# Optimization experiments

Hardware: AMD Instinct MI355X
Metric: run time of the kernel (lower is better)

## Reference

```python
import jax, jax.numpy as jnp
import numpy as np

B, N, H, T = 64, 64, 128, 128


def setup_inputs() -> dict:
    key = jax.random.key(0)
    ks = jax.random.split(key, 8)
    tf = jax.random.normal(ks[0], (B, N, H, T), dtype=jnp.float32)
    # learnable symmetric adjacency parameter
    ap = jax.random.normal(ks[1], (N, N), dtype=jnp.float32) * 0.1
    ap = (ap + ap.T) / 2
    # edge MLP params (stored as (in, out) for x @ W)
    W1 = jax.random.normal(ks[2], (2 * H, H), dtype=jnp.float32) * (1.0 / np.sqrt(2 * H))
    b1 = jnp.zeros((H,), dtype=jnp.float32)
    W2 = jax.random.normal(ks[3], (H, H // 2), dtype=jnp.float32) * (1.0 / np.sqrt(H))
    b2 = jnp.zeros((H // 2,), dtype=jnp.float32)
    W3 = jax.random.normal(ks[4], (H // 2, 1), dtype=jnp.float32) * (1.0 / np.sqrt(H // 2))
    b3 = jnp.zeros((1,), dtype=jnp.float32)
    return {"temporal_features": tf, "adj_param": ap, "W1": W1, "b1": b1,
            "W2": W2, "b2": b2, "W3": W3, "b3": b3}


def reference(temporal_features, adj_param, W1, b1, W2, b2, W3, b3):
    # node features: mean over time -> (B, N, H)
    node = temporal_features.mean(axis=-1)
    h_dim = node.shape[-1]
    # concat([h_i, h_j]) @ W1 == h_i @ W1[:H] + h_j @ W1[H:]  (avoids materializing 2H concat)
    Wi, Wj = W1[:h_dim], W1[h_dim:]
    pi = jnp.einsum('bnh,hk->bnk', node, Wi)  # (B, N, H)
    pj = jnp.einsum('bnh,hk->bnk', node, Wj)
    h = jax.nn.relu(pi[:, :, None, :] + pj[:, None, :, :] + b1)  # (B, N, N, H)
    # Dropout(0.2) is identity at inference
    h = jax.nn.relu(jnp.einsum('bijh,hk->bijk', h, W2) + b2)      # (B, N, N, H//2)
    feat_adj = (jnp.einsum('bijk,ko->bijo', h, W3) + b3)[..., 0]  # (B, N, N)
    # combined method
    adj = 0.5 * adj_param[None, :, :] + 0.5 * feat_adj
    # symmetrize + relu
    adj = jax.nn.relu((adj + jnp.swapaxes(adj, -2, -1)) / 2)
    # add self-loops and degree-normalize rows
    adj = adj + jnp.eye(adj.shape[-1], dtype=adj.dtype)[None]
    adj = adj / (adj.sum(axis=-1, keepdims=True) + 1e-8)
    return adj
```

## Files before the change

### kernel.cpp

```cpp
#include <hip/hip_runtime.h>
#include <stdint.h>
#include <stddef.h>

typedef __attribute__((ext_vector_type(8))) short short8;
typedef __attribute__((ext_vector_type(4))) float f32x4;

__device__ inline unsigned short f2bf(float x) {
    unsigned u = __float_as_uint(x);
    unsigned r = (u + 0x7fffu + ((u >> 16) & 1u)) >> 16;
    return (unsigned short)r;
}

__global__ __launch_bounds__(256) void k1_mean(const float* __restrict__ tf,
                                               float* __restrict__ node) {
    int wave = (blockIdx.x * blockDim.x + threadIdx.x) >> 6;
    int lane = threadIdx.x & 63;
    int half = lane >> 5;
    int c = lane & 31;
    const float4* tf4 = reinterpret_cast<const float4*>(tf);
    size_t base = (size_t)wave * 8 * 64;

    float4 v[8];
#pragma unroll
    for (int k = 0; k < 8; ++k) v[k] = tf4[base + (size_t)k * 64 + lane];

    float s[8];
#pragma unroll
    for (int k = 0; k < 8; ++k) s[k] = (v[k].x + v[k].y) + (v[k].z + v[k].w);
#pragma unroll
    for (int m = 1; m <= 16; m <<= 1) {
#pragma unroll
        for (int k = 0; k < 8; ++k) s[k] += __shfl_xor(s[k], m);
    }
    if (c == 0) {
#pragma unroll
        for (int k = 0; k < 8; ++k) {
            int rp = wave * 8 + k;
            node[(size_t)rp * 2 + half] = s[k] * (1.0f / 128.0f);
        }
    }
}

__global__ __launch_bounds__(256) void k2_proj(const float* __restrict__ node,
                                               const float* __restrict__ W1,
                                               const float* __restrict__ b1,
                                               float* __restrict__ pi,
                                               float* __restrict__ pj) {
    const int LP = 136;
    __shared__ unsigned short A_lds[32 * LP];
    __shared__ unsigned short BT[128 * LP];
    __shared__ float b1s[128];

    int tid = threadIdx.x;
    int rblk = blockIdx.x >> 1;
    int half = blockIdx.x & 1;
    int r0 = rblk * 32;

    {
        int row = tid >> 3;
        int c0 = (tid & 7) * 16;
        const float4* src = reinterpret_cast<const float4*>(node + (size_t)(r0 + row) * 128 + c0);
        short8 pk[2];
#pragma unroll
        for (int q = 0; q < 2; ++q) {
            float4 va = src[q * 2 + 0];
            float4 vb = src[q * 2 + 1];
            pk[q][0] = (short)f2bf(va.x); pk[q][1] = (short)f2bf(va.y);
            pk[q][2] = (short)f2bf(va.z); pk[q][3] = (short)f2bf(va.w);
            pk[q][4] = (short)f2bf(vb.x); pk[q][5] = (short)f2bf(vb.y);
            pk[q][6] = (short)f2bf(vb.z); pk[q][7] = (short)f2bf(vb.w);
        }
        short8* dst = reinterpret_cast<short8*>(&A_lds[row * LP + c0]);
        dst[0] = pk[0];
        dst[1] = pk[1];
    }
    {
        int n = tid & 127;
        int kh = tid >> 7;
        const float* Wbase = W1 + (size_t)half * 128 * 128 + n;
#pragma unroll
        for (int g = 0; g < 8; ++g) {
            int kb = kh * 64 + g * 8;
            short8 pk;
#pragma unroll
            for (int e = 0; e < 8; ++e) pk[e] = (short)f2bf(Wbase[(size_t)(kb + e) * 128]);
            *reinterpret_cast<short8*>(&BT[n * LP + kb]) = pk;
        }
    }
    if (tid < 128) b1s[tid] = b1[tid];
    __syncthreads();

    int w = tid >> 6;
    int l = tid & 63;
    int lr = l & 15;
    int lg = l >> 4;
    int rt = w & 1;
    int ch = w >> 1;

    f32x4 acc[4] = {{0,0,0,0},{0,0,0,0},{0,0,0,0},{0,0,0,0}};
#pragma unroll
    for (int ks = 0; ks < 4; ++ks) {
        int kb = ks * 32 + lg * 8;
        short8 afrag = *reinterpret_cast<const short8*>(&A_lds[(rt * 16 + lr) * LP + kb]);
#pragma unroll
        for (int nt = 0; nt < 4; ++nt) {
            short8 bfrag = *reinterpret_cast<const short8*>(&BT[(ch * 64 + nt * 16 + lr) * LP + kb]);
            acc[nt] = __builtin_amdgcn_mfma_f32_16x16x32_bf16(afrag, bfrag, acc[nt], 0, 0, 0);
        }
    }
    float* out = half ? pj : pi;
#pragma unroll
    for (int nt = 0; nt < 4; ++nt) {
        int col = ch * 64 + nt * 16 + lr;
        float bias = half ? 0.0f : b1s[col];
#pragma unroll
        for (int r = 0; r < 4; ++r) {
            int row = r0 + rt * 16 + lg * 4 + r;
            out[(size_t)row * 128 + col] = acc[nt][r] + bias;
        }
    }
}

__global__ __launch_bounds__(256) void k3_mlp(const float* __restrict__ pi,
                                              const float* __restrict__ pj,
                                              const float* __restrict__ W2,
                                              const float* __restrict__ b2,
                                              const float* __restrict__ W3,
                                              const float* __restrict__ b3,
                                              float* __restrict__ F) {
    const int LDA = 136;
    __shared__ unsigned short A_lds[64 * LDA];
    __shared__ unsigned short W2T[64 * LDA];
    __shared__ float pipb4[4][128];
    __shared__ float b2s[64], w3s[64];

    int tid = threadIdx.x;
    int b = blockIdx.x >> 4;
    int it = blockIdx.x & 15;
    int i0 = it * 4;
    int jt = tid >> 2;
    int kq = tid & 3;

    float pjreg[32];
    {
        const float* src = pj + ((size_t)(b * 64 + jt) * 128 + kq * 32);
#pragma unroll
        for (int e = 0; e < 8; ++e) {
            float4 v = reinterpret_cast<const float4*>(src)[e];
            pjreg[e * 4 + 0] = v.x;
            pjreg[e * 4 + 1] = v.y;
            pjreg[e * 4 + 2] = v.z;
            pjreg[e * 4 + 3] = v.w;
        }
    }
    if (tid < 128) {
        int row = tid >> 5;
        int c4 = tid & 31;
        float4 v = reinterpret_cast<const float4*>(pi + ((size_t)(b * 64 + i0 + row) * 128))[c4];
        reinterpret_cast<float4*>(&pipb4[row][0])[c4] = v;
    }
    {
        int m = jt;
        for (int e = 0; e < 32; ++e) {
            int k = kq * 32 + e;
            W2T[m * LDA + k] = f2bf(W2[(size_t)k * 64 + m]);
        }
    }
    if (tid < 64) {
        b2s[tid] = b2[tid];
        w3s[tid] = W3[tid];
    }
    float b3v = b3[0];
    __syncthreads();

    int w = tid >> 6;
    int l = tid & 63;
    int lr = l & 15;
    int lg = l >> 4;

    for (int il = 0; il < 4; ++il) {
        {
            unsigned* dst = reinterpret_cast<unsigned*>(&A_lds[jt * LDA + kq * 32]);
#pragma unroll
            for (int e2 = 0; e2 < 16; ++e2) {
                float a0 = pipb4[il][kq * 32 + e2 * 2 + 0] + pjreg[e2 * 2 + 0];
                float a1 = pipb4[il][kq * 32 + e2 * 2 + 1] + pjreg[e2 * 2 + 1];
                a0 = fmaxf(a0, 0.0f);
                a1 = fmaxf(a1, 0.0f);
                dst[e2] = (unsigned)f2bf(a0) | ((unsigned)f2bf(a1) << 16);
            }
        }
        __syncthreads();
        f32x4 acc0 = {0.f, 0.f, 0.f, 0.f};
        f32x4 acc1 = {0.f, 0.f, 0.f, 0.f};
        f32x4 acc2 = {0.f, 0.f, 0.f, 0.f};
        f32x4 acc3 = {0.f, 0.f, 0.f, 0.f};
#pragma unroll
        for (int ks = 0; ks < 4; ++ks) {
            int kb = ks * 32 + lg * 8;
            short8 afrag = *reinterpret_cast<const short8*>(&A_lds[(w * 16 + lr) * LDA + kb]);
            short8 b0 = *reinterpret_cast<const short8*>(&W2T[(0 * 16 + lr) * LDA + kb]);
            short8 b1f = *reinterpret_cast<const short8*>(&W2T[(1 * 16 + lr) * LDA + kb]);
            short8 b2f = *reinterpret_cast<const short8*>(&W2T[(2 * 16 + lr) * LDA + kb]);
            short8 b3f = *reinterpret_cast<const short8*>(&W2T[(3 * 16 + lr) * LDA + kb]);
            acc0 = __builtin_amdgcn_mfma_f32_16x16x32_bf16(afrag, b0, acc0, 0, 0, 0);
            acc1 = __builtin_amdgcn_mfma_f32_16x16x32_bf16(afrag, b1f, acc1, 0, 0, 0);
            acc2 = __builtin_amdgcn_mfma_f32_16x16x32_bf16(afrag, b2f, acc2, 0, 0, 0);
            acc3 = __builtin_amdgcn_mfma_f32_16x16x32_bf16(afrag, b3f, acc3, 0, 0, 0);
        }
        float part[4] = {0.f, 0.f, 0.f, 0.f};
#pragma unroll
        for (int mt = 0; mt < 4; ++mt) {
            int m = mt * 16 + lr;
            float w3 = w3s[m];
            float bb = b2s[m];
            f32x4 a = (mt == 0) ? acc0 : (mt == 1) ? acc1 : (mt == 2) ? acc2 : acc3;
#pragma unroll
            for (int r = 0; r < 4; ++r) {
                float h = fmaxf(a[r] + bb, 0.0f);
                part[r] += h * w3;
            }
        }
#pragma unroll
        for (int r = 0; r < 4; ++r) {
            part[r] += __shfl_xor(part[r], 1);
            part[r] += __shfl_xor(part[r], 2);
            part[r] += __shfl_xor(part[r], 4);
            part[r] += __shfl_xor(part[r], 8);
        }
        if (lr == 0) {
#pragma unroll
            for (int r = 0; r < 4; ++r) {
                int j = w * 16 + lg * 4 + r;
                F[((size_t)b * 64 + i0 + il) * 64 + j] = part[r] + b3v;
            }
        }
        __syncthreads();
    }
}

__global__ __launch_bounds__(256) void k4_final(const float* __restrict__ F,
                                                const float* __restrict__ ap,
                                                float* __restrict__ out) {
    __shared__ float s[64][65];
    __shared__ float rs[64];
    int b = blockIdx.x;
    int tid = threadIdx.x;
    for (int idx = tid; idx < 4096; idx += 256) {
        int i = idx >> 6, j = idx & 63;
        float f_ij = F[(size_t)b * 4096 + idx];
        float f_ji = F[(size_t)b * 4096 + j * 64 + i];
        float a_ij = ap[idx];
        float a_ji = ap[j * 64 + i];
        float v = 0.25f * (a_ij + a_ji) + 0.25f * (f_ij + f_ji);
        v = fmaxf(v, 0.0f);
        if (i == j) v += 1.0f;
        s[i][j] = v;
    }
    __syncthreads();
    int wv = tid >> 6, ln = tid & 63;
    for (int i = wv * 16; i < wv * 16 + 16; ++i) {
        float v = s[i][ln];
        v += __shfl_xor(v, 1);
        v += __shfl_xor(v, 2);
        v += __shfl_xor(v, 4);
        v += __shfl_xor(v, 8);
        v += __shfl_xor(v, 16);
        v += __shfl_xor(v, 32);
        if (ln == 0) rs[i] = v;
    }
    __syncthreads();
    for (int idx = tid; idx < 4096; idx += 256) {
        int i = idx >> 6, j = idx & 63;
        out[(size_t)b * 4096 + idx] = s[i][j] / (rs[i] + 1e-8f);
    }
}

extern "C" void kernel_launch(void* const* d_in, const int* in_sizes, int n_in,
                              void* d_out, int out_size, void* d_ws, size_t ws_size,
                              hipStream_t stream) {
    const float* tf = (const float*)d_in[0];
    const float* ap = (const float*)d_in[1];
    const float* W1 = (const float*)d_in[2];
    const float* b1 = (const float*)d_in[3];
    const float* W2 = (const float*)d_in[4];
    const float* b2 = (const float*)d_in[5];
    const float* W3 = (const float*)d_in[6];
    const float* b3 = (const float*)d_in[7];
    float* out = (float*)d_out;

    char* ws = (char*)d_ws;
    float* node = (float*)(ws);
    float* pi   = (float*)(ws + (size_t)(2 << 20));
    float* pj   = (float*)(ws + (size_t)(4 << 20));
    float* F    = (float*)(ws + (size_t)(6 << 20));

    k1_mean<<<8192, 256, 0, stream>>>(tf, node);
    k2_proj<<<256, 256, 0, stream>>>(node, W1, b1, pi, pj);
    k3_mlp<<<1024, 256, 0, stream>>>(pi, pj, W2, b2, W3, b3, F);
    k4_final<<<64, 256, 0, stream>>>(F, ap, out);
}
```

Measured before the change: 77.07 us.

## Fuse temporal mean and W1 projection into a single kernel

Merges the time-mean reduction and the bf16 MFMA projection into one kernel of 512 blocks by 512 threads. Each block reduces 8 node rows straight into LDS as bf16 and then computes both the pi and pj halves, so the node buffer is never written to or read from global memory. This also removes one kernel launch. In exchange, every block converts the full 256x128 W1 to bf16 (redundant work across blocks), uses a much larger LDS footprint, and pads an 8-row tile to 16 rows, which wastes half of the MFMA work.

```diff
diff --git a/kernel.cpp b/kernel.cpp
--- a/kernel.cpp
+++ b/kernel.cpp
@@ -11,112 +11,92 @@
     return (unsigned short)r;
 }
 
-__global__ __launch_bounds__(256) void k1_mean(const float* __restrict__ tf,
-                                               float* __restrict__ node) {
-    int wave = (blockIdx.x * blockDim.x + threadIdx.x) >> 6;
-    int lane = threadIdx.x & 63;
-    int half = lane >> 5;
-    int c = lane & 31;
-    const float4* tf4 = reinterpret_cast<const float4*>(tf);
-    size_t base = (size_t)wave * 8 * 64;
-
-    float4 v[8];
-#pragma unroll
-    for (int k = 0; k < 8; ++k) v[k] = tf4[base + (size_t)k * 64 + lane];
-
-    float s[8];
-#pragma unroll
-    for (int k = 0; k < 8; ++k) s[k] = (v[k].x + v[k].y) + (v[k].z + v[k].w);
-#pragma unroll
-    for (int m = 1; m <= 16; m <<= 1) {
-#pragma unroll
-        for (int k = 0; k < 8; ++k) s[k] += __shfl_xor(s[k], m);
-    }
-    if (c == 0) {
-#pragma unroll
-        for (int k = 0; k < 8; ++k) {
-            int rp = wave * 8 + k;
-            node[(size_t)rp * 2 + half] = s[k] * (1.0f / 128.0f);
-        }
-    }
-}
-
-__global__ __launch_bounds__(256) void k2_proj(const float* __restrict__ node,
-                                               const float* __restrict__ W1,
-                                               const float* __restrict__ b1,
-                                               float* __restrict__ pi,
-                                               float* __restrict__ pj) {
+__global__ __launch_bounds__(512) void k12_mean_proj(const float* __restrict__ tf,
+                                                     const float* __restrict__ W1,
+                                                     const float* __restrict__ b1,
+                                                     float* __restrict__ pi,
+                                                     float* __restrict__ pj) {
     const int LP = 136;
-    __shared__ unsigned short A_lds[32 * LP];
-    __shared__ unsigned short BT[128 * LP];
+    __shared__ unsigned short A_lds[16 * LP];
+    __shared__ unsigned short BT[256 * LP];
     __shared__ float b1s[128];
 
     int tid = threadIdx.x;
-    int rblk = blockIdx.x >> 1;
-    int half = blockIdx.x & 1;
-    int r0 = rblk * 32;
+    int blk = blockIdx.x;
+    int R0 = blk * 8;
+
+    for (int idx = tid; idx < 16 * LP; idx += 512) A_lds[idx] = 0;
 
     {
-        int row = tid >> 3;
-        int c0 = (tid & 7) * 16;
-        const float4* src = reinterpret_cast<const float4*>(node + (size_t)(r0 + row) * 128 + c0);
-        short8 pk[2];
-#pragma unroll
-        for (int q = 0; q < 2; ++q) {
-            float4 va = src[q * 2 + 0];
-            float4 vb = src[q * 2 + 1];
-            pk[q][0] = (short)f2bf(va.x); pk[q][1] = (short)f2bf(va.y);
-            pk[q][2] = (short)f2bf(va.z); pk[q][3] = (short)f2bf(va.w);
-            pk[q][4] = (short)f2bf(vb.x); pk[q][5] = (short)f2bf(vb.y);
-            pk[q][6] = (short)f2bf(vb.z); pk[q][7] = (short)f2bf(vb.w);
-        }
-        short8* dst = reinterpret_cast<short8*>(&A_lds[row * LP + c0]);
-        dst[0] = pk[0];
-        dst[1] = pk[1];
-    }
-    {
-        int n = tid & 127;
-        int kh = tid >> 7;
-        const float* Wbase = W1 + (size_t)half * 128 * 128 + n;
+        int c = tid & 255;
+        int kh = tid >> 8;
+        int n = c & 127, hf = c >> 7;
+        const float* Wb = W1 + (size_t)hf * 128 * 128 + n;
 #pragma unroll
         for (int g = 0; g < 8; ++g) {
             int kb = kh * 64 + g * 8;
             short8 pk;
 #pragma unroll
-            for (int e = 0; e < 8; ++e) pk[e] = (short)f2bf(Wbase[(size_t)(kb + e) * 128]);
-            *reinterpret_cast<short8*>(&BT[n * LP + kb]) = pk;
+            for (int e = 0; e < 8; ++e) pk[e] = (short)f2bf(Wb[(size_t)(kb + e) * 128]);
+            *reinterpret_cast<short8*>(&BT[c * LP + kb]) = pk;
         }
     }
     if (tid < 128) b1s[tid] = b1[tid];
-    __syncthreads();
 
     int w = tid >> 6;
     int l = tid & 63;
-    int lr = l & 15;
-    int lg = l >> 4;
-    int rt = w & 1;
-    int ch = w >> 1;
-
-    f32x4 acc[4] = {{0,0,0,0},{0,0,0,0},{0,0,0,0},{0,0,0,0}};
+    int half = l >> 5;
+    int c32 = l & 31;
+    const float4* tf4 = reinterpret_cast<const float4*>(tf);
+    size_t bb = (size_t)blk * 32768;
+
+    for (int it = 0; it < 8; ++it) {
+        float4 v[8];
+#pragma unroll
+        for (int k = 0; k < 8; ++k) {
+            int rp = w * 64 + it * 8 + k;
+            v[k] = tf4[bb + (size_t)rp * 64 + l];
+        }
+        float s[8];
+#pragma unroll
+        for (int k = 0; k < 8; ++k) s[k] = (v[k].x + v[k].y) + (v[k].z + v[k].w);
+#pragma unroll
+        for (int m = 1; m <= 16; m <<= 1) {
+#pragma unroll
+            for (int k = 0; k < 8; ++k) s[k] += __shfl_xor(s[k], m);
+        }
+        if (c32 == 0) {
+#pragma unroll
+            for (int k = 0; k < 8; ++k) {
+                int tr = (w * 64 + it * 8 + k) * 2 + half;
+                A_lds[(tr >> 7) * LP + (tr & 127)] = f2bf(s[k] * (1.0f / 128.0f));
+            }
+        }
+    }
+    __syncthreads();
+
+    int lr = l & 15, lg = l >> 4;
+    f32x4 acc[2] = {{0, 0, 0, 0}, {0, 0, 0, 0}};
 #pragma unroll
     for (int ks = 0; ks < 4; ++ks) {
         int kb = ks * 32 + lg * 8;
-        short8 afrag = *reinterpret_cast<const short8*>(&A_lds[(rt * 16 + lr) * LP + kb]);
-#pragma unroll
-        for (int nt = 0; nt < 4; ++nt) {
-            short8 bfrag = *reinterpret_cast<const short8*>(&BT[(ch * 64 + nt * 16 + lr) * LP + kb]);
-            acc[nt] = __builtin_amdgcn_mfma_f32_16x16x32_bf16(afrag, bfrag, acc[nt], 0, 0, 0);
-        }
-    }
-    float* out = half ? pj : pi;
-#pragma unroll
-    for (int nt = 0; nt < 4; ++nt) {
-        int col = ch * 64 + nt * 16 + lr;
-        float bias = half ? 0.0f : b1s[col];
-#pragma unroll
-        for (int r = 0; r < 4; ++r) {
-            int row = r0 + rt * 16 + lg * 4 + r;
-            out[(size_t)row * 128 + col] = acc[nt][r] + bias;
+        short8 af = *reinterpret_cast<const short8*>(&A_lds[lr * LP + kb]);
+#pragma unroll
+        for (int nt = 0; nt < 2; ++nt) {
+            short8 bf = *reinterpret_cast<const short8*>(&BT[(w * 32 + nt * 16 + lr) * LP + kb]);
+            acc[nt] = __builtin_amdgcn_mfma_f32_16x16x32_bf16(af, bf, acc[nt], 0, 0, 0);
+        }
+    }
+    if (lg < 2) {
+#pragma unroll
+        for (int nt = 0; nt < 2; ++nt) {
+            int col = w * 32 + nt * 16 + lr;
+#pragma unroll
+            for (int r = 0; r < 4; ++r) {
+                int row = R0 + lg * 4 + r;
+                if (col < 128) pi[(size_t)row * 128 + col] = acc[nt][r] + b1s[col];
+                else           pj[(size_t)row * 128 + (col - 128)] = acc[nt][r];
+            }
         }
     }
 }
@@ -290,13 +270,11 @@
     float* out = (float*)d_out;
 
     char* ws = (char*)d_ws;
-    float* node = (float*)(ws);
     float* pi   = (float*)(ws + (size_t)(2 << 20));
     float* pj   = (float*)(ws + (size_t)(4 << 20));
     float* F    = (float*)(ws + (size_t)(6 << 20));
 
-    k1_mean<<<8192, 256, 0, stream>>>(tf, node);
-    k2_proj<<<256, 256, 0, stream>>>(node, W1, b1, pi, pj);
+    k12_mean_proj<<<512, 512, 0, stream>>>(tf, W1, b1, pi, pj);
     k3_mlp<<<1024, 256, 0, stream>>>(pi, pj, W2, b2, W3, b3, F);
     k4_final<<<64, 256, 0, stream>>>(F, ap, out);
 }
```

Result: slower. 78.99 us (+2.5%).
